# Performance work log

Measured on AMD Instinct MI355X. Metric: run time of the kernel, lower is better.

The kernel has to match this reference:

```python
import jax, jax.numpy as jnp
import numpy as np

B, K, C = 8, 16384, 256
NPROP, NSAMPLE, RADIUS = 1024, 16, 0.3
NUM_CLASS, NH, NS = 18, 12, 18
DOUT = 2 + 3 + NH * 2 + NS * 4 + NUM_CLASS  # 119


def setup_inputs() -> dict:
    key = jax.random.key(0)
    ks = jax.random.split(key, 16)
    w = lambda k, shape: jax.random.normal(k, shape, jnp.float32) * 0.05
    return {
        "xyz": jax.random.uniform(ks[0], (B, K, 3), jnp.float32) * 4.0,
        "features": jax.random.normal(ks[1], (B, C, K), jnp.float32),
        # SA shared-MLP (conv2d 1x1) weights, BN folded to scale/bias (inference)
        "W1": w(ks[2], (128, C + 3)), "g1": jnp.ones((128,), jnp.float32), "b1": jnp.zeros((128,), jnp.float32),
        "W2": w(ks[3], (128, 128)),   "g2": jnp.ones((128,), jnp.float32), "b2": jnp.zeros((128,), jnp.float32),
        "W3": w(ks[4], (128, 128)),   "g3": jnp.ones((128,), jnp.float32), "b3": jnp.zeros((128,), jnp.float32),
        # proposal head conv1d stack
        "P1": w(ks[5], (128, 128)),  "pg1": jnp.ones((128,), jnp.float32), "pb1": jnp.zeros((128,), jnp.float32),
        "P2": w(ks[6], (128, 128)),  "pg2": jnp.ones((128,), jnp.float32), "pb2": jnp.zeros((128,), jnp.float32),
        "P3": w(ks[7], (DOUT, 128)), "pb3": jnp.zeros((DOUT,), jnp.float32),
        "mean_size_arr": jnp.abs(jax.random.normal(ks[8], (NS, 3), jnp.float32)) + 0.5,
    }


def fps(xyz, npoint):
    """Farthest point sampling. xyz: [B,K,3] -> [B,npoint] int32."""
    Bn, Kn, _ = xyz.shape
    def step(carry, _):
        dist, far = carry                                   # [B,K], [B]
        sel = jnp.take_along_axis(xyz, far[:, None, None], axis=1)  # [B,1,3]
        d = jnp.sum((xyz - sel) ** 2, axis=-1)              # [B,K]
        dist = jnp.minimum(dist, d)
        return (dist, jnp.argmax(dist, axis=-1).astype(jnp.int32)), far
    init = (jnp.full((Bn, Kn), 1e10, xyz.dtype), jnp.zeros((Bn,), jnp.int32))
    _, inds = jax.lax.scan(step, init, None, length=npoint)  # [npoint,B]
    return inds.T


def ball_query(new_xyz, xyz, radius, nsample):
    """First nsample points within radius of each center (pad with first hit)."""
    Kn = xyz.shape[1]
    d2 = jnp.sum((new_xyz[:, :, None, :] - xyz[:, None, :, :]) ** 2, axis=-1)  # [B,P,K]
    idx = jnp.where(d2 < radius * radius, jnp.arange(Kn, dtype=jnp.int32)[None, None, :], Kn)
    idx = jnp.sort(idx, axis=-1)[..., :nsample]             # first hits in index order
    first = idx[..., :1]                                    # center itself is always a hit
    return jnp.where(idx == Kn, first, idx).astype(jnp.int32)


def reference(xyz, features, W1, g1, b1, W2, g2, b2, W3, g3, b3,
              P1, pg1, pb1, P2, pg2, pb2, P3, pb3, mean_size_arr):
    Bn = xyz.shape[0]
    fps_idx = fps(xyz, NPROP)                                           # [B,P]
    new_xyz = jnp.take_along_axis(xyz, fps_idx[:, :, None], axis=1)     # [B,P,3]
    idx = ball_query(new_xyz, xyz, RADIUS, NSAMPLE)                     # [B,P,S]
    flat = idx.reshape(Bn, -1)
    g_xyz = jnp.take_along_axis(xyz, flat[:, :, None], axis=1).reshape(Bn, NPROP, NSAMPLE, 3)
    g_xyz = (g_xyz - new_xyz[:, :, None, :]) / RADIUS                   # normalize_xyz=True
    f = jnp.swapaxes(features, 1, 2)                                    # [B,K,C]
    g_feat = jnp.take_along_axis(f, flat[:, :, None], axis=1).reshape(Bn, NPROP, NSAMPLE, C)
    x = jnp.concatenate([g_xyz, g_feat], axis=-1)                       # [B,P,S,C+3] (use_xyz)
    for Wl, gl, bl in ((W1, g1, b1), (W2, g2, b2), (W3, g3, b3)):
        x = jax.nn.relu(jnp.einsum('bpsc,oc->bpso', x, Wl) * gl + bl)
    feat = jnp.max(x, axis=2)                                           # [B,P,128] max-pool over ball
    h = jax.nn.relu(jnp.einsum('bpc,oc->bpo', feat, P1) * pg1 + pb1)
    h = jax.nn.relu(jnp.einsum('bpc,oc->bpo', h, P2) * pg2 + pb2)
    net = jnp.einsum('bpc,oc->bpo', h, P3) + pb3                        # [B,P,119]
    # decode_scores slicing
    obj = net[:, :, 0:2]
    center = new_xyz + net[:, :, 2:5]
    heading_scores = net[:, :, 5:5 + NH]
    heading_residuals = net[:, :, 5 + NH:5 + 2 * NH] * (np.pi / NH)
    size_scores = net[:, :, 5 + 2 * NH:5 + 2 * NH + NS]
    srn = net[:, :, 5 + 2 * NH + NS:5 + 2 * NH + 4 * NS].reshape(Bn, NPROP, NS, 3)
    size_residuals = srn * mean_size_arr[None, None]
    sem_cls_scores = net[:, :, 5 + 2 * NH + 4 * NS:]
    return (obj, center, heading_scores, heading_residuals, size_scores,
            size_residuals, sem_cls_scores, feat)
```

## Files before the change

kernel.cpp:

```cpp
#include <hip/hip_runtime.h>
#include <math.h>

static constexpr int BB = 8;
static constexpr int KK = 16384;
static constexpr int CC = 256;
static constexpr int NPROP = 1024;
static constexpr int NSAMP = 16;
static constexpr int NH = 12;
static constexpr int NS = 18;
static constexpr int NCLS = 18;
static constexpr int DOUT = 119;
static constexpr int NTT = 8192;
static constexpr int NPREP = 112;

static constexpr int OFF_OBJ = 0;
static constexpr int OFF_CEN = OFF_OBJ + BB * NPROP * 2;
static constexpr int OFF_HS  = OFF_CEN + BB * NPROP * 3;
static constexpr int OFF_HR  = OFF_HS + BB * NPROP * NH;
static constexpr int OFF_SS  = OFF_HR + BB * NPROP * NH;
static constexpr int OFF_SR  = OFF_SS + BB * NPROP * NS;
static constexpr int OFF_SC  = OFF_SR + BB * NPROP * NS * 3;
static constexpr int OFF_FEAT = OFF_SC + BB * NPROP * NCLS;

__global__ __launch_bounds__(1024, 4) void stage1(
    const float* __restrict__ xyz, const float* __restrict__ features,
    const float* __restrict__ W1, const float* __restrict__ W2, const float* __restrict__ W3,
    const float* __restrict__ P1, const float* __restrict__ P2, const float* __restrict__ P3,
    float* __restrict__ fT, float* __restrict__ W1T, float* __restrict__ W2T,
    float* __restrict__ W3T, float* __restrict__ P1T, float* __restrict__ P2T,
    float* __restrict__ P3T, float* __restrict__ new_xyz) {
#pragma clang fp contract(off)
    __shared__ union {
        float t[64 * 65];
        struct { float redv[32]; int redi[32]; } r;
    } sm;
    int tid = threadIdx.x;
    int blk = blockIdx.x;

    if (blk < BB) {
        const int b = blk;
        const int lane = tid & 63, wid = tid >> 6;
        const float* xb = xyz + (size_t)b * KK * 3;

        float px[16], py[16], pz[16], dist[16];
#pragma unroll
        for (int j = 0; j < 16; j++) {
            int idx = j * 1024 + tid;
            px[j] = xb[idx * 3 + 0];
            py[j] = xb[idx * 3 + 1];
            pz[j] = xb[idx * 3 + 2];
            dist[j] = 1e10f;
        }
        float sx = xb[0], sy = xb[1], sz = xb[2];
        for (int t = 0; t < NPROP; t++) {
            if (tid == 0) {
                size_t o = ((size_t)b * NPROP + t) * 3;
                new_xyz[o + 0] = sx;
                new_xyz[o + 1] = sy;
                new_xyz[o + 2] = sz;
            }
#pragma unroll
            for (int j = 0; j < 16; j++)
                asm volatile("" : "+v"(px[j]), "+v"(py[j]), "+v"(pz[j]));
            float lmax = -1.f;
            int lidx = 0;
#pragma unroll
            for (int j = 0; j < 16; j++) {
                float dx = px[j] - sx;
                float dy = py[j] - sy;
                float dz = pz[j] - sz;
                float a = dx * dx;
                float bq = dy * dy;
                float cq = dz * dz;
                float d = (a + bq) + cq;
                float nd = dist[j] < d ? dist[j] : d;
                dist[j] = nd;
                if (nd > lmax) { lmax = nd; lidx = j * 1024 + tid; }
            }
#pragma unroll
            for (int m = 1; m < 64; m <<= 1) {
                float ov = __shfl_xor(lmax, m, 64);
                int oi = __shfl_xor(lidx, m, 64);
                if (ov > lmax || (ov == lmax && oi < lidx)) { lmax = ov; lidx = oi; }
            }
            int buf = (t & 1) * 16;
            if (lane == 0) { sm.r.redv[buf + wid] = lmax; sm.r.redi[buf + wid] = lidx; }
            __syncthreads();
            float v = sm.r.redv[buf + (lane & 15)];
            int i2 = sm.r.redi[buf + (lane & 15)];
#pragma unroll
            for (int m = 1; m < 16; m <<= 1) {
                float ov = __shfl_xor(v, m, 64);
                int oi = __shfl_xor(i2, m, 64);
                if (ov > v || (ov == v && oi < i2)) { v = ov; i2 = oi; }
            }
            int cs = __builtin_amdgcn_readfirstlane(i2);
            sx = xb[cs * 3 + 0];
            sy = xb[cs * 3 + 1];
            sz = xb[cs * 3 + 2];
        }
        return;
    }
    blk -= BB;

    if (blk < NTT) {
        int bz = blk >> 10;
        int t2 = blk & 1023;
        int k0 = (t2 & 255) << 6;
        int c0 = (t2 >> 8) << 6;
        int tx = tid & 63, ty = tid >> 6;
        const float* fb = features + (size_t)bz * CC * KK;
#pragma unroll
        for (int i = 0; i < 4; i++) {
            int c = ty + (i << 4);
            sm.t[c * 65 + tx] = fb[(size_t)(c0 + c) * KK + k0 + tx];
        }
        __syncthreads();
        float* fTb = fT + (size_t)bz * KK * CC;
#pragma unroll
        for (int i = 0; i < 4; i++) {
            int k = ty + (i << 4);
            fTb[(size_t)(k0 + k) * CC + c0 + tx] = sm.t[tx * 65 + k];
        }
        return;
    }
    blk -= NTT;

    {
        int i = blk * 1024 + tid;
        if (i < 260 * 128) {
            int c = i >> 7, o = i & 127;
            W1T[i] = (c < 259) ? W1[o * 259 + c] : 0.f;
            return;
        }
        i -= 260 * 128;
        if (i < 16384) { int c = i >> 7, o = i & 127; W2T[i] = W2[o * 128 + c]; return; }
        i -= 16384;
        if (i < 16384) { int c = i >> 7, o = i & 127; W3T[i] = W3[o * 128 + c]; return; }
        i -= 16384;
        if (i < 16384) { int c = i >> 7, o = i & 127; P1T[i] = P1[o * 128 + c]; return; }
        i -= 16384;
        if (i < 16384) { int c = i >> 7, o = i & 127; P2T[i] = P2[o * 128 + c]; return; }
        i -= 16384;
        if (i < 128 * DOUT) { int c = i / DOUT, o = i % DOUT; P3T[i] = P3[o * 128 + c]; return; }
    }
}

__global__ __launch_bounds__(256) void ballquery_kernel(const float* __restrict__ xyz,
                                                        const float* __restrict__ new_xyz,
                                                        int* __restrict__ bq) {
#pragma clang fp contract(off)
    int gid = blockIdx.x * 4 + (threadIdx.x >> 6);
    int lane = threadIdx.x & 63;
    int b = gid >> 10, p = gid & 1023;
    const float* xb = xyz + (size_t)b * KK * 3;
    float cx = new_xyz[(b * NPROP + p) * 3 + 0];
    float cy = new_xyz[(b * NPROP + p) * 3 + 1];
    float cz = new_xyz[(b * NPROP + p) * 3 + 2];
    const float R2 = (float)(0.3 * 0.3);
    int out_base = (b * NPROP + p) * NSAMP;
    int found = 0;
    int firsthit = -1;
    for (int base = 0; base < KK && found < NSAMP; base += 64) {
        int k = base + lane;
        float dx = cx - xb[k * 3 + 0];
        float dy = cy - xb[k * 3 + 1];
        float dz = cz - xb[k * 3 + 2];
        float a = dx * dx;
        float bb2 = dy * dy;
        float cc2 = dz * dz;
        float d2 = (a + bb2) + cc2;
        bool pred = d2 < R2;
        unsigned long long mask = __ballot(pred);
        int prefix = __popcll(mask & ((1ull << lane) - 1ull));
        if (pred) {
            int pos = found + prefix;
            if (pos < NSAMP) bq[out_base + pos] = k;
        }
        if (firsthit < 0 && mask) firsthit = base + (__ffsll(mask) - 1);
        found += __popcll(mask);
    }
    if (lane < NSAMP && lane >= found) bq[out_base + lane] = firsthit;
}

__global__ __launch_bounds__(256) void fused_mlp(
    const float* __restrict__ fT, const float* __restrict__ xyz,
    const float* __restrict__ new_xyz, const int* __restrict__ bq,
    const float* __restrict__ W1T, const float* __restrict__ g1, const float* __restrict__ b1,
    const float* __restrict__ W2T, const float* __restrict__ g2, const float* __restrict__ b2,
    const float* __restrict__ W3T, const float* __restrict__ g3, const float* __restrict__ b3,
    const float* __restrict__ P1T, const float* __restrict__ pg1, const float* __restrict__ pb1,
    const float* __restrict__ P2T, const float* __restrict__ pg2, const float* __restrict__ pb2,
    const float* __restrict__ P3T, const float* __restrict__ pb3, const float* __restrict__ msa,
    float* __restrict__ out) {
    __shared__ float xs[16][260];
    __shared__ float hA[16][128];
    __shared__ float hB[16][128];
    __shared__ float pmax[8][128];
    __shared__ float featl[128];
    __shared__ float heada[128];
    __shared__ float headb[128];
    __shared__ int sidx[16];

    int tid = threadIdx.x;
    int blk = blockIdx.x;
    int b = blk >> 10, p = blk & 1023;
    int bp = b * NPROP + p;

    if (tid < 16) sidx[tid] = bq[bp * NSAMP + tid];
    float c0 = new_xyz[bp * 3 + 0];
    float c1 = new_xyz[bp * 3 + 1];
    float c2 = new_xyz[bp * 3 + 2];
    __syncthreads();

    for (int s = 0; s < 16; s++) {
        int k = sidx[s];
        xs[s][3 + tid] = fT[((size_t)(b * KK + k)) * CC + tid];
        if (tid < 3) {
            float xv = xyz[((size_t)(b * KK + k)) * 3 + tid];
            float cv = (tid == 0) ? c0 : (tid == 1) ? c1 : c2;
            xs[s][tid] = (xv - cv) / 0.3f;
        }
        if (tid == 3) xs[s][259] = 0.f;
    }
    __syncthreads();

    int og = tid & 31, sg = tid >> 5;
    int o0 = og * 4, s0 = sg * 2;
    float acc[4][2];

#pragma unroll
    for (int oi = 0; oi < 4; oi++) { acc[oi][0] = 0.f; acc[oi][1] = 0.f; }
    for (int cg = 0; cg < 65; cg++) {
        int cb = cg * 4;
        float wv[4][4], xv[2][4];
#pragma unroll
        for (int j = 0; j < 4; j++)
            *(float4*)&wv[j][0] = *(const float4*)&W1T[(cb + j) * 128 + o0];
        *(float4*)&xv[0][0] = *(const float4*)&xs[s0][cb];
        *(float4*)&xv[1][0] = *(const float4*)&xs[s0 + 1][cb];
#pragma unroll
        for (int j = 0; j < 4; j++)
#pragma unroll
            for (int oi = 0; oi < 4; oi++) {
                acc[oi][0] += wv[j][oi] * xv[0][j];
                acc[oi][1] += wv[j][oi] * xv[1][j];
            }
    }
    {
        float ga[4], ba[4];
        *(float4*)ga = *(const float4*)&g1[o0];
        *(float4*)ba = *(const float4*)&b1[o0];
#pragma unroll
        for (int si = 0; si < 2; si++) {
            float tmp[4];
#pragma unroll
            for (int oi = 0; oi < 4; oi++)
                tmp[oi] = fmaxf(acc[oi][si] * ga[oi] + ba[oi], 0.f);
            *(float4*)&hA[s0 + si][o0] = *(float4*)tmp;
        }
    }
    __syncthreads();

#pragma unroll
    for (int oi = 0; oi < 4; oi++) { acc[oi][0] = 0.f; acc[oi][1] = 0.f; }
    for (int cg = 0; cg < 32; cg++) {
        int cb = cg * 4;
        float wv[4][4], xv[2][4];
#pragma unroll
        for (int j = 0; j < 4; j++)
            *(float4*)&wv[j][0] = *(const float4*)&W2T[(cb + j) * 128 + o0];
        *(float4*)&xv[0][0] = *(const float4*)&hA[s0][cb];
        *(float4*)&xv[1][0] = *(const float4*)&hA[s0 + 1][cb];
#pragma unroll
        for (int j = 0; j < 4; j++)
#pragma unroll
            for (int oi = 0; oi < 4; oi++) {
                acc[oi][0] += wv[j][oi] * xv[0][j];
                acc[oi][1] += wv[j][oi] * xv[1][j];
            }
    }
    {
        float ga[4], ba[4];
        *(float4*)ga = *(const float4*)&g2[o0];
        *(float4*)ba = *(const float4*)&b2[o0];
#pragma unroll
        for (int si = 0; si < 2; si++) {
            float tmp[4];
#pragma unroll
            for (int oi = 0; oi < 4; oi++)
                tmp[oi] = fmaxf(acc[oi][si] * ga[oi] + ba[oi], 0.f);
            *(float4*)&hB[s0 + si][o0] = *(float4*)tmp;
        }
    }
    __syncthreads();

#pragma unroll
    for (int oi = 0; oi < 4; oi++) { acc[oi][0] = 0.f; acc[oi][1] = 0.f; }
    for (int cg = 0; cg < 32; cg++) {
        int cb = cg * 4;
        float wv[4][4], xv[2][4];
#pragma unroll
        for (int j = 0; j < 4; j++)
            *(float4*)&wv[j][0] = *(const float4*)&W3T[(cb + j) * 128 + o0];
        *(float4*)&xv[0][0] = *(const float4*)&hB[s0][cb];
        *(float4*)&xv[1][0] = *(const float4*)&hB[s0 + 1][cb];
#pragma unroll
        for (int j = 0; j < 4; j++)
#pragma unroll
            for (int oi = 0; oi < 4; oi++) {
                acc[oi][0] += wv[j][oi] * xv[0][j];
                acc[oi][1] += wv[j][oi] * xv[1][j];
            }
    }
    {
        float ga[4], ba[4];
        *(float4*)ga = *(const float4*)&g3[o0];
        *(float4*)ba = *(const float4*)&b3[o0];
        float tmp[4];
#pragma unroll
        for (int oi = 0; oi < 4; oi++) {
            float v0 = fmaxf(acc[oi][0] * ga[oi] + ba[oi], 0.f);
            float v1 = fmaxf(acc[oi][1] * ga[oi] + ba[oi], 0.f);
            tmp[oi] = fmaxf(v0, v1);
        }
        *(float4*)&pmax[sg][o0] = *(float4*)tmp;
    }
    __syncthreads();

    if (tid < 128) {
        float m = pmax[0][tid];
#pragma unroll
        for (int s = 1; s < 8; s++) m = fmaxf(m, pmax[s][tid]);
        featl[tid] = m;
        out[OFF_FEAT + (size_t)bp * 128 + tid] = m;
    }
    __syncthreads();

    if (tid < 128) {
        float s = 0.f;
        for (int c = 0; c < 128; c++) s += P1T[c * 128 + tid] * featl[c];
        heada[tid] = fmaxf(s * pg1[tid] + pb1[tid], 0.f);
    }
    __syncthreads();
    if (tid < 128) {
        float s = 0.f;
        for (int c = 0; c < 128; c++) s += P2T[c * 128 + tid] * heada[c];
        headb[tid] = fmaxf(s * pg2[tid] + pb2[tid], 0.f);
    }
    __syncthreads();
    if (tid < DOUT) {
        float s = 0.f;
        for (int c = 0; c < 128; c++) s += P3T[c * DOUT + tid] * headb[c];
        s += pb3[tid];
        if (tid < 2) {
            out[OFF_OBJ + (size_t)bp * 2 + tid] = s;
        } else if (tid < 5) {
            out[OFF_CEN + (size_t)bp * 3 + (tid - 2)] = new_xyz[bp * 3 + (tid - 2)] + s;
        } else if (tid < 17) {
            out[OFF_HS + (size_t)bp * NH + (tid - 5)] = s;
        } else if (tid < 29) {
            out[OFF_HR + (size_t)bp * NH + (tid - 17)] = s * (float)(M_PI / 12.0);
        } else if (tid < 47) {
            out[OFF_SS + (size_t)bp * NS + (tid - 29)] = s;
        } else if (tid < 101) {
            int j = tid - 47;
            out[OFF_SR + (size_t)bp * NS * 3 + j] = s * msa[j];
        } else {
            out[OFF_SC + (size_t)bp * NCLS + (tid - 101)] = s;
        }
    }
}

extern "C" void kernel_launch(void* const* d_in, const int* in_sizes, int n_in,
                              void* d_out, int out_size, void* d_ws, size_t ws_size,
                              hipStream_t stream) {
    const float* xyz = (const float*)d_in[0];
    const float* features = (const float*)d_in[1];
    const float* W1 = (const float*)d_in[2];
    const float* g1 = (const float*)d_in[3];
    const float* b1 = (const float*)d_in[4];
    const float* W2 = (const float*)d_in[5];
    const float* g2 = (const float*)d_in[6];
    const float* b2 = (const float*)d_in[7];
    const float* W3 = (const float*)d_in[8];
    const float* g3 = (const float*)d_in[9];
    const float* b3 = (const float*)d_in[10];
    const float* P1 = (const float*)d_in[11];
    const float* pg1 = (const float*)d_in[12];
    const float* pb1 = (const float*)d_in[13];
    const float* P2 = (const float*)d_in[14];
    const float* pg2 = (const float*)d_in[15];
    const float* pb2 = (const float*)d_in[16];
    const float* P3 = (const float*)d_in[17];
    const float* pb3 = (const float*)d_in[18];
    const float* msa = (const float*)d_in[19];
    float* out = (float*)d_out;

    char* w = (char*)d_ws;
    float* W1T = (float*)w; w += (size_t)260 * 128 * 4;
    float* W2T = (float*)w; w += 16384 * 4;
    float* W3T = (float*)w; w += 16384 * 4;
    float* P1T = (float*)w; w += 16384 * 4;
    float* P2T = (float*)w; w += 16384 * 4;
    float* P3T = (float*)w; w += 16384 * 4;
    float* nxyz = (float*)w; w += (size_t)BB * NPROP * 3 * 4;
    int* bq = (int*)w;     w += (size_t)BB * NPROP * NSAMP * 4;
    float* fT = (float*)w; w += (size_t)BB * KK * CC * 4;

    stage1<<<BB + NTT + NPREP, 1024, 0, stream>>>(
        xyz, features, W1, W2, W3, P1, P2, P3,
        fT, W1T, W2T, W3T, P1T, P2T, P3T, nxyz);
    ballquery_kernel<<<(BB * NPROP) / 4, 256, 0, stream>>>(xyz, nxyz, bq);
    fused_mlp<<<BB * NPROP, 256, 0, stream>>>(
        fT, xyz, nxyz, bq,
        W1T, g1, b1, W2T, g2, b2, W3T, g3, b3,
        P1T, pg1, pb1, P2T, pg2, pb2, P3T, pb3, msa, out);
}
```

Measured before the change: 3.625 ms.

## Stage FPS point coordinates in LDS instead of registers

The farthest-point-sampling blocks now keep 12K of the 16K points per batch in shared memory (xy interleaved plus z) and only 4 points per thread in registers, cutting VGPR pressure so the kernel can hold a waves-per-EU target of 4. The selected point's coordinates are read from LDS when possible rather than global memory. The cost is about 147KB of dynamic LDS for every block of stage1, including the transpose and prep blocks. That likely limits co-residency of those many transpose blocks, and each FPS iteration now issues extra LDS reads.

```diff
diff --git a/kernel.cpp b/kernel.cpp
--- a/kernel.cpp
+++ b/kernel.cpp
@@ -13,6 +13,11 @@
 static constexpr int NTT = 8192;
 static constexpr int NPREP = 112;
 
+static constexpr int LP = 12288;
+static constexpr int RPT = 4;
+static constexpr int DSM_FLOATS = 3 * LP + 64;
+static constexpr size_t DSM_BYTES = DSM_FLOATS * 4;
+
 static constexpr int OFF_OBJ = 0;
 static constexpr int OFF_CEN = OFF_OBJ + BB * NPROP * 2;
 static constexpr int OFF_HS  = OFF_CEN + BB * NPROP * 3;
@@ -22,7 +27,8 @@
 static constexpr int OFF_SC  = OFF_SR + BB * NPROP * NS * 3;
 static constexpr int OFF_FEAT = OFF_SC + BB * NPROP * NCLS;
 
-__global__ __launch_bounds__(1024, 4) void stage1(
+__global__ __launch_bounds__(1024) __attribute__((amdgpu_waves_per_eu(4, 4)))
+void stage1(
     const float* __restrict__ xyz, const float* __restrict__ features,
     const float* __restrict__ W1, const float* __restrict__ W2, const float* __restrict__ W3,
     const float* __restrict__ P1, const float* __restrict__ P2, const float* __restrict__ P3,
@@ -30,10 +36,7 @@
     float* __restrict__ W3T, float* __restrict__ P1T, float* __restrict__ P2T,
     float* __restrict__ P3T, float* __restrict__ new_xyz) {
 #pragma clang fp contract(off)
-    __shared__ union {
-        float t[64 * 65];
-        struct { float redv[32]; int redi[32]; } r;
-    } sm;
+    extern __shared__ float dsm[];
     int tid = threadIdx.x;
     int blk = blockIdx.x;
 
@@ -42,16 +45,32 @@
         const int lane = tid & 63, wid = tid >> 6;
         const float* xb = xyz + (size_t)b * KK * 3;
 
-        float px[16], py[16], pz[16], dist[16];
-#pragma unroll
-        for (int j = 0; j < 16; j++) {
-            int idx = j * 1024 + tid;
-            px[j] = xb[idx * 3 + 0];
-            py[j] = xb[idx * 3 + 1];
-            pz[j] = xb[idx * 3 + 2];
-            dist[j] = 1e10f;
-        }
+        float* xy = dsm;
+        float* zs = dsm + 2 * LP;
+        float* redv = dsm + 3 * LP;
+        int* redi = (int*)(dsm + 3 * LP + 32);
+
+#pragma unroll
+        for (int j = 0; j < 12; j++) {
+            int p = j * 1024 + tid;
+            xy[2 * p]     = xb[p * 3 + 0];
+            xy[2 * p + 1] = xb[p * 3 + 1];
+            zs[p]         = xb[p * 3 + 2];
+        }
+        float rx[RPT], ry[RPT], rz[RPT];
+#pragma unroll
+        for (int j = 0; j < RPT; j++) {
+            int p = LP + j * 1024 + tid;
+            rx[j] = xb[p * 3 + 0];
+            ry[j] = xb[p * 3 + 1];
+            rz[j] = xb[p * 3 + 2];
+        }
+        float dist[16];
+#pragma unroll
+        for (int j = 0; j < 16; j++) dist[j] = 1e10f;
         float sx = xb[0], sy = xb[1], sz = xb[2];
+        __syncthreads();
+
         for (int t = 0; t < NPROP; t++) {
             if (tid == 0) {
                 size_t o = ((size_t)b * NPROP + t) * 3;
@@ -59,23 +78,39 @@
                 new_xyz[o + 1] = sy;
                 new_xyz[o + 2] = sz;
             }
-#pragma unroll
-            for (int j = 0; j < 16; j++)
-                asm volatile("" : "+v"(px[j]), "+v"(py[j]), "+v"(pz[j]));
+            asm volatile("" : "+v"(rx[0]), "+v"(rx[1]), "+v"(rx[2]), "+v"(rx[3]),
+                             "+v"(ry[0]), "+v"(ry[1]), "+v"(ry[2]), "+v"(ry[3]),
+                             "+v"(rz[0]), "+v"(rz[1]), "+v"(rz[2]), "+v"(rz[3]));
             float lmax = -1.f;
             int lidx = 0;
 #pragma unroll
-            for (int j = 0; j < 16; j++) {
-                float dx = px[j] - sx;
-                float dy = py[j] - sy;
-                float dz = pz[j] - sz;
+            for (int j = 0; j < 12; j++) {
+                int p = j * 1024 + tid;
+                float2 v = *(const float2*)&xy[2 * p];
+                float z = zs[p];
+                float dx = v.x - sx;
+                float dy = v.y - sy;
+                float dz = z - sz;
                 float a = dx * dx;
                 float bq = dy * dy;
                 float cq = dz * dz;
                 float d = (a + bq) + cq;
                 float nd = dist[j] < d ? dist[j] : d;
                 dist[j] = nd;
-                if (nd > lmax) { lmax = nd; lidx = j * 1024 + tid; }
+                if (nd > lmax) { lmax = nd; lidx = p; }
+            }
+#pragma unroll
+            for (int j = 0; j < RPT; j++) {
+                float dx = rx[j] - sx;
+                float dy = ry[j] - sy;
+                float dz = rz[j] - sz;
+                float a = dx * dx;
+                float bq = dy * dy;
+                float cq = dz * dz;
+                float d = (a + bq) + cq;
+                float nd = dist[12 + j] < d ? dist[12 + j] : d;
+                dist[12 + j] = nd;
+                if (nd > lmax) { lmax = nd; lidx = LP + j * 1024 + tid; }
             }
 #pragma unroll
             for (int m = 1; m < 64; m <<= 1) {
@@ -84,10 +119,10 @@
                 if (ov > lmax || (ov == lmax && oi < lidx)) { lmax = ov; lidx = oi; }
             }
             int buf = (t & 1) * 16;
-            if (lane == 0) { sm.r.redv[buf + wid] = lmax; sm.r.redi[buf + wid] = lidx; }
+            if (lane == 0) { redv[buf + wid] = lmax; redi[buf + wid] = lidx; }
             __syncthreads();
-            float v = sm.r.redv[buf + (lane & 15)];
-            int i2 = sm.r.redi[buf + (lane & 15)];
+            float v = redv[buf + (lane & 15)];
+            int i2 = redi[buf + (lane & 15)];
 #pragma unroll
             for (int m = 1; m < 16; m <<= 1) {
                 float ov = __shfl_xor(v, m, 64);
@@ -95,9 +130,14 @@
                 if (ov > v || (ov == v && oi < i2)) { v = ov; i2 = oi; }
             }
             int cs = __builtin_amdgcn_readfirstlane(i2);
-            sx = xb[cs * 3 + 0];
-            sy = xb[cs * 3 + 1];
-            sz = xb[cs * 3 + 2];
+            if (cs < LP) {
+                float2 sv = *(const float2*)&xy[2 * cs];
+                sx = sv.x; sy = sv.y; sz = zs[cs];
+            } else {
+                sx = xb[cs * 3 + 0];
+                sy = xb[cs * 3 + 1];
+                sz = xb[cs * 3 + 2];
+            }
         }
         return;
     }
@@ -113,14 +153,14 @@
 #pragma unroll
         for (int i = 0; i < 4; i++) {
             int c = ty + (i << 4);
-            sm.t[c * 65 + tx] = fb[(size_t)(c0 + c) * KK + k0 + tx];
+            dsm[c * 65 + tx] = fb[(size_t)(c0 + c) * KK + k0 + tx];
         }
         __syncthreads();
         float* fTb = fT + (size_t)bz * KK * CC;
 #pragma unroll
         for (int i = 0; i < 4; i++) {
             int k = ty + (i << 4);
-            fTb[(size_t)(k0 + k) * CC + c0 + tx] = sm.t[tx * 65 + k];
+            fTb[(size_t)(k0 + k) * CC + c0 + tx] = dsm[tx * 65 + k];
         }
         return;
     }
@@ -408,7 +448,11 @@
     int* bq = (int*)w;     w += (size_t)BB * NPROP * NSAMP * 4;
     float* fT = (float*)w; w += (size_t)BB * KK * CC * 4;
 
-    stage1<<<BB + NTT + NPREP, 1024, 0, stream>>>(
+    hipFuncSetAttribute((const void*)stage1,
+                        hipFuncAttributeMaxDynamicSharedMemorySize,
+                        (int)DSM_BYTES);
+
+    stage1<<<BB + NTT + NPREP, 1024, DSM_BYTES, stream>>>(
         xyz, features, W1, W2, W3, P1, P2, P3,
         fT, W1T, W2T, W3T, P1T, P2T, P3T, nxyz);
     ballquery_kernel<<<(BB * NPROP) / 4, 256, 0, stream>>>(xyz, nxyz, bq);
```

Measured after the change: 3.358 ms. 7.4% less time.
